# Kernel optimization log

Measured on AMD Instinct MI355X. Metric: run time of the kernel, lower is better.

## Reference

```python
import jax, jax.numpy as jnp
import numpy as np

DIM = 4096
N_HEAD = 32
N_KV_HEAD = 8
HEAD_DIM = DIM // N_HEAD  # 128
B, T = 2, 2048


def _rope_freqs(T, head_dim, theta=10000.0):
    inv = 1.0 / (theta ** (np.arange(0, head_dim, 2, dtype=np.float32) / head_dim))
    t = np.arange(T, dtype=np.float32)
    ang = np.outer(t, inv)  # [T, head_dim/2]
    return jnp.asarray(np.stack([np.cos(ang), np.sin(ang)], axis=-1))  # [T, hd/2, 2]


def setup_inputs() -> dict:
    key = jax.random.key(0)
    ks = jax.random.split(key, 5)
    s = 1.0 / np.sqrt(DIM)
    return {
        "x": jax.random.normal(ks[0], (B, T, DIM), dtype=jnp.float32),
        "freqs_cis": _rope_freqs(T, HEAD_DIM),
        "wq": jax.random.normal(ks[1], (DIM, N_HEAD * HEAD_DIM), dtype=jnp.float32) * s,
        "wk": jax.random.normal(ks[2], (DIM, N_KV_HEAD * HEAD_DIM), dtype=jnp.float32) * s,
        "wv": jax.random.normal(ks[3], (DIM, N_KV_HEAD * HEAD_DIM), dtype=jnp.float32) * s,
        "wo": jax.random.normal(ks[4], (DIM, DIM), dtype=jnp.float32) * s,
    }


def _apply_rotary(x, freqs_cis):
    # x: [B, T, H, head_dim]; freqs_cis: [T, head_dim/2, 2]
    xs = x.reshape(*x.shape[:-1], -1, 2)  # [B, T, H, hd/2, 2]
    fc = freqs_cis[None, :, None, :, :]   # [1, T, 1, hd/2, 2]
    real = xs[..., 0] * fc[..., 0] - xs[..., 1] * fc[..., 1]
    imag = xs[..., 1] * fc[..., 0] + xs[..., 0] * fc[..., 1]
    return jnp.stack([real, imag], axis=-1).reshape(x.shape)


def reference(x, freqs_cis, wq, wk, wv, wo):
    Bx, Tx, C = x.shape
    q = (x @ wq).reshape(Bx, Tx, N_HEAD, HEAD_DIM)
    k = (x @ wk).reshape(Bx, Tx, N_KV_HEAD, HEAD_DIM)
    v = (x @ wv).reshape(Bx, Tx, N_KV_HEAD, HEAD_DIM)
    q = _apply_rotary(q, freqs_cis)
    k = _apply_rotary(k, freqs_cis)
    # [B, H, T, hd]
    q = q.transpose(0, 2, 1, 3)
    k = k.transpose(0, 2, 1, 3)
    v = v.transpose(0, 2, 1, 3)
    # GQA: expand kv heads to match query heads
    rep = N_HEAD // N_KV_HEAD
    k = jnp.repeat(k, rep, axis=1)
    v = jnp.repeat(v, rep, axis=1)
    scale = 1.0 / np.sqrt(HEAD_DIM)
    scores = jnp.einsum("bhqd,bhkd->bhqk", q, k) * scale
    causal = jnp.tril(jnp.ones((Tx, Tx), dtype=bool))
    scores = jnp.where(causal[None, None], scores, jnp.float32(-1e30))
    attn = jax.nn.softmax(scores, axis=-1)
    y = jnp.einsum("bhqk,bhkd->bhqd", attn, v)
    y = y.transpose(0, 2, 1, 3).reshape(Bx, Tx, C)
    return y @ wo
```

## Files before the change

### kernel.cpp

```cpp
#include <hip/hip_runtime.h>

#define DIM  4096
#define NH   32
#define NKV  8
#define HD   128
#define BSZ  2
#define TSEQ 2048

typedef __bf16 bf16x8 __attribute__((ext_vector_type(8)));
typedef unsigned short ushort8v __attribute__((ext_vector_type(8)));
typedef float f32x4 __attribute__((ext_vector_type(4)));

typedef void GV __attribute__((address_space(1)));
typedef void LV __attribute__((address_space(3)));

__device__ __forceinline__ unsigned short f2bf(float f) {
  unsigned u = __builtin_bit_cast(unsigned, f);
  u += 0x7FFFu + ((u >> 16) & 1u);
  return (unsigned short)(u >> 16);
}
__device__ __forceinline__ float bf2f(unsigned short b) {
  unsigned u = ((unsigned)b) << 16;
  return __builtin_bit_cast(float, u);
}
__device__ __forceinline__ void gload16(const unsigned short* g, unsigned short* l) {
  __builtin_amdgcn_global_load_lds((GV*)g, (LV*)l, 16, 0, 0);
}
__device__ __forceinline__ f32x4 mfma16(bf16x8 a, bf16x8 b, f32x4 c) {
  return __builtin_amdgcn_mfma_f32_16x16x32_bf16(a, b, c, 0, 0, 0);
}
__device__ __forceinline__ bf16x8 lds8(const unsigned short* p) {
  return __builtin_bit_cast(bf16x8, *(const ushort8v*)p);
}

__global__ void detect_dtype(const unsigned int* __restrict__ fc, int* __restrict__ flag) {
  if (threadIdx.x == 0 && blockIdx.x == 0)
    *flag = (fc[0] == 0x3F800000u) ? 0 : 1;
}

__global__ void cast_x(const void* __restrict__ src, unsigned short* __restrict__ dst,
                       const int* __restrict__ flag) {
  long t = (long)blockIdx.x * 256 + threadIdx.x;
  if (*flag) {
    ((uint2*)dst)[t] = ((const uint2*)src)[t];
  } else {
    float4 f = ((const float4*)src)[t];
    ushort4 o;
    o.x = f2bf(f.x); o.y = f2bf(f.y); o.z = f2bf(f.z); o.w = f2bf(f.w);
    ((ushort4*)dst)[t] = o;
  }
}

__global__ __launch_bounds__(256) void transpose64(const void* __restrict__ src,
                                                   unsigned short* __restrict__ dst,
                                                   int R, int C, const int* __restrict__ flag) {
  __shared__ unsigned short tile[64][68];
  const int isbf = *flag;
  const int tid = threadIdx.x;
  const int c0g = blockIdx.x * 64, r0g = blockIdx.y * 64;
  const int cc = (tid & 15) * 4;
  if (isbf) {
    const unsigned short* s = (const unsigned short*)src;
#pragma unroll
    for (int it = 0; it < 4; ++it) {
      const int r = it * 16 + (tid >> 4);
      ushort4 v = *(const ushort4*)(s + (long)(r0g + r) * C + c0g + cc);
      *(ushort4*)&tile[r][cc] = v;
    }
  } else {
    const float* s = (const float*)src;
#pragma unroll
    for (int it = 0; it < 4; ++it) {
      const int r = it * 16 + (tid >> 4);
      float4 f = *(const float4*)(s + (long)(r0g + r) * C + c0g + cc);
      ushort4 v;
      v.x = f2bf(f.x); v.y = f2bf(f.y); v.z = f2bf(f.z); v.w = f2bf(f.w);
      *(ushort4*)&tile[r][cc] = v;
    }
  }
  __syncthreads();
#pragma unroll
  for (int it = 0; it < 2; ++it) {
    const int c = (tid >> 3) + it * 32;
    const int r0 = (tid & 7) * 8;
    ushort8v o;
#pragma unroll
    for (int u = 0; u < 8; ++u) o[u] = tile[r0 + u][c];
    *(ushort8v*)(dst + (long)(c0g + c) * R + r0g + r0) = o;
  }
}

__device__ __forceinline__ void gemm128_loop(const unsigned short* __restrict__ A,
                                             const unsigned short* __restrict__ Bt,
                                             unsigned short* As, unsigned short* Bs,
                                             long tileM, long tileN, f32x4 (&acc)[4][4]) {
  const int tid = (int)threadIdx.x;
  const int lane = tid & 63, wave = tid >> 6;
  const int wr = wave >> 1, wc = wave & 1;
  const int lm = lane & 15, quad = lane >> 4;
  const int sr = tid >> 3;
  const int schunk = ((tid & 7) ^ (sr & 7)) * 8;
  const unsigned short* Ag = A + (tileM + sr) * 4096L + schunk;
  const unsigned short* Bg = Bt + (tileN + sr) * 4096L + schunk;
  unsigned short* Al = As + sr * 64 + (tid & 7) * 8;
  unsigned short* Bl = Bs + sr * 64 + (tid & 7) * 8;

  auto stgA = [&](int slot, int half, int tt) {
    const unsigned short* g = Ag + (long)half * (64 * 4096L) + (long)tt * 64;
    unsigned short* l = Al + slot * 8192 + half * 4096;
    gload16(g, l);
    gload16(g + 32 * 4096L, l + 2048);
  };
  auto stgB = [&](int slot, int half, int tt) {
    const unsigned short* g = Bg + (long)half * (64 * 4096L) + (long)tt * 64;
    unsigned short* l = Bl + slot * 8192 + half * 4096;
    gload16(g, l);
    gload16(g + 32 * 4096L, l + 2048);
  };
  auto rdA = [&](int so, int f, int kk) {
    return lds8(&As[so + (wr * 64 + f * 16 + lm) * 64 + (((kk * 4 + quad) ^ (lm & 7)) * 8)]);
  };
  auto rdB = [&](int so, int f, int kk) {
    return lds8(&Bs[so + (wc * 64 + f * 16 + lm) * 64 + (((kk * 4 + quad) ^ (lm & 7)) * 8)]);
  };

  stgB(0, 0, 0); stgB(0, 1, 0); stgA(0, 0, 0); stgA(0, 1, 0);
  stgB(1, 0, 1); stgB(1, 1, 1); stgA(1, 0, 1);
  asm volatile("s_waitcnt vmcnt(6)" ::: "memory");
  __builtin_amdgcn_sched_barrier(0);
  __builtin_amdgcn_s_barrier();

#pragma unroll 2
  for (int t = 0; t < 64; ++t) {
    __builtin_amdgcn_sched_barrier(0);
    const int s = t & 1;
    const int so = s * 8192;
    bf16x8 a[4][2], b[4][2];
#pragma unroll
    for (int f = 0; f < 4; ++f) { a[f][0] = rdA(so, f, 0); a[f][1] = rdA(so, f, 1); }
#pragma unroll
    for (int f = 0; f < 4; ++f) { b[f][0] = rdB(so, f, 0); b[f][1] = rdB(so, f, 1); }
    if (t < 63) stgA(s ^ 1, 1, t + 1);
    asm volatile("s_waitcnt lgkmcnt(0)" ::: "memory");
    __builtin_amdgcn_sched_barrier(0);
    __builtin_amdgcn_s_setprio(1);
#pragma unroll
    for (int mf = 0; mf < 4; ++mf)
#pragma unroll
      for (int nf = 0; nf < 4; ++nf)
        acc[mf][nf] = mfma16(a[mf][0], b[nf][0], acc[mf][nf]);
    __builtin_amdgcn_s_setprio(0);
    __builtin_amdgcn_sched_barrier(0);
    __builtin_amdgcn_s_barrier();
    if (t < 62) { stgB(s, 0, t + 2); stgB(s, 1, t + 2); stgA(s, 0, t + 2); }
    __builtin_amdgcn_s_setprio(1);
#pragma unroll
    for (int mf = 0; mf < 4; ++mf)
#pragma unroll
      for (int nf = 0; nf < 4; ++nf)
        acc[mf][nf] = mfma16(a[mf][1], b[nf][1], acc[mf][nf]);
    __builtin_amdgcn_s_setprio(0);
    if (t < 62)       asm volatile("s_waitcnt vmcnt(6)" ::: "memory");
    else if (t == 62) asm volatile("s_waitcnt vmcnt(0)" ::: "memory");
    __builtin_amdgcn_sched_barrier(0);
    __builtin_amdgcn_s_barrier();
  }
}

__global__ __launch_bounds__(256, 2) void gemm_qkv8(const unsigned short* __restrict__ A,
                                                    const unsigned short* __restrict__ Bt,
                                                    const void* __restrict__ fcv,
                                                    const int* __restrict__ flag,
                                                    unsigned short* __restrict__ qo,
                                                    unsigned short* __restrict__ ko,
                                                    unsigned short* __restrict__ vo) {
  __shared__ __align__(16) unsigned short As[2 * 8192];
  __shared__ __align__(16) unsigned short Bs[2 * 8192];
  const int bid = (int)blockIdx.x;
  const int nb2 = (bid & 7) * 192 + (bid >> 3);
  const long tileM = (long)(nb2 / 48) * 128;
  const long tileN = (long)(nb2 % 48) * 128;
  f32x4 acc[4][4] = {};
  gemm128_loop(A, Bt, As, Bs, tileM, tileN, acc);
  const int tid = (int)threadIdx.x;
  const int lane = tid & 63, wave = tid >> 6;
  const int wr = wave >> 1, wc = wave & 1;
  const int lm = lane & 15, quad = lane >> 4;
  const int isbf = *flag;
  const int nb = (int)tileN + wc * 64;
  if (nb < 5120) {
    const int isk = (nb >= 4096);
    unsigned short* dst = isk ? ko : qo;
    const int hpb = isk ? NKV : NH;
    const int coff = isk ? 4096 : 0;
#pragma unroll
    for (int mf = 0; mf < 4; ++mf)
#pragma unroll
      for (int r = 0; r < 4; ++r) {
        const int m = (int)tileM + wr * 64 + mf * 16 + quad * 4 + r;
        const int b = m >> 11, tq = m & (TSEQ - 1);
#pragma unroll
        for (int nf = 0; nf < 4; ++nf) {
          const int n = nb + nf * 16 + lm;
          float val = acc[mf][nf][r];
          float par = __shfl_xor(val, 1);
          const int ip = (n & 127) >> 1;
          const long fo = (long)tq * 64 + ip;
          float cz, sz;
          if (isbf) {
            const unsigned short* fu = (const unsigned short*)fcv;
            cz = bf2f(fu[fo * 2]); sz = bf2f(fu[fo * 2 + 1]);
          } else {
            float2 cs = ((const float2*)fcv)[fo];
            cz = cs.x; sz = cs.y;
          }
          float out = (n & 1) ? (val * cz + par * sz) : (val * cz - par * sz);
          const int h = (n - coff) >> 7, d = n & 127;
          dst[((long)(b * hpb + h) * TSEQ + tq) * HD + d] = f2bf(out);
        }
      }
  } else {
#pragma unroll
    for (int mf = 0; mf < 4; ++mf)
#pragma unroll
      for (int r = 0; r < 4; ++r) {
        const int m = (int)tileM + wr * 64 + mf * 16 + quad * 4 + r;
        const int b = m >> 11, tq = m & (TSEQ - 1);
#pragma unroll
        for (int nf = 0; nf < 4; ++nf) {
          const int n = nb + nf * 16 + lm;
          const int h = (n - 5120) >> 7, d = n & 127;
          vo[((long)(b * NKV + h) * HD + d) * TSEQ + tq] = f2bf(acc[mf][nf][r]);
        }
      }
  }
}

__global__ __launch_bounds__(256, 2) void gemm_wo8(const unsigned short* __restrict__ A,
                                                   const unsigned short* __restrict__ Bt,
                                                   void* __restrict__ Cv,
                                                   const int* __restrict__ flag) {
  __shared__ __align__(16) unsigned short As[2 * 8192];
  __shared__ __align__(16) unsigned short Bs[2 * 8192];
  const int bid = (int)blockIdx.x;
  const int nb2 = (bid & 7) * 128 + (bid >> 3);
  const long tileM = (long)(nb2 >> 5) * 128;
  const long tileN = (long)(nb2 & 31) * 128;
  f32x4 acc[4][4] = {};
  gemm128_loop(A, Bt, As, Bs, tileM, tileN, acc);
  const int tid = (int)threadIdx.x;
  const int lane = tid & 63, wave = tid >> 6;
  const int wr = wave >> 1, wc = wave & 1;
  const int lm = lane & 15, quad = lane >> 4;
  const int obf = *flag;
  const long N = 4096;
  if (obf) {
    unsigned short* C = (unsigned short*)Cv;
#pragma unroll
    for (int mf = 0; mf < 4; ++mf)
#pragma unroll
      for (int nf = 0; nf < 4; ++nf)
#pragma unroll
        for (int r = 0; r < 4; ++r)
          C[(tileM + wr * 64 + mf * 16 + quad * 4 + r) * N + tileN + wc * 64 + nf * 16 + lm] =
              f2bf(acc[mf][nf][r]);
  } else {
    float* C = (float*)Cv;
#pragma unroll
    for (int mf = 0; mf < 4; ++mf)
#pragma unroll
      for (int nf = 0; nf < 4; ++nf)
#pragma unroll
        for (int r = 0; r < 4; ++r)
          C[(tileM + wr * 64 + mf * 16 + quad * 4 + r) * N + tileN + wc * 64 + nf * 16 + lm] =
              acc[mf][nf][r];
  }
}

__global__ __launch_bounds__(256, 3) void flash_attn(const unsigned short* __restrict__ q,
                                                     const unsigned short* __restrict__ k,
                                                     const unsigned short* __restrict__ vT,
                                                     unsigned short* __restrict__ y) {
  __shared__ unsigned short Ks[2][32 * 128];
  __shared__ unsigned short Vs[2][128 * 32];
  __shared__ unsigned short Pl[4][32 * 40];
  const int tid = threadIdx.x;
  const int lane = tid & 63, wave = tid >> 6;
  const int lm = lane & 15, quad = lane >> 4;
  const int bh = blockIdx.y, b = bh >> 5, h = bh & 31, kvh = h >> 2;
  const int pr = (int)blockIdx.x;
  const unsigned short* Kb = k + (long)(b * NKV + kvh) * TSEQ * HD;
  const unsigned short* Vb = vT + (long)(b * NKV + kvh) * HD * TSEQ;
  const float scale = 0.08838834764831845f;
  const int krow = tid >> 4, kcl = ((tid & 15) ^ (krow & 7)) * 8;
  const int vrow = tid >> 2, vcl = ((tid & 3) ^ ((vrow >> 1) & 3)) * 8;

  for (int seg = 0; seg < 2; ++seg) {
    const int qi = seg ? (15 - pr) : pr;
    const int q0 = qi * 128;
    const unsigned short* Qb = q + ((long)(b * NH + h) * TSEQ + q0 + wave * 32) * HD;
    bf16x8 qf[2][4];
#pragma unroll
    for (int mi = 0; mi < 2; ++mi)
#pragma unroll
      for (int ks = 0; ks < 4; ++ks)
        qf[mi][ks] = __builtin_bit_cast(bf16x8,
            *(const ushort8v*)(Qb + (mi * 16 + lm) * HD + ks * 32 + quad * 8));
    f32x4 o[2][8] = {};
    float li[2][4] = {};
    const int ktiles = qi * 4 + 4;
    if (seg) __syncthreads();
    {
      gload16(Kb + krow * HD + kcl, &Ks[0][tid * 8]);
      gload16(Kb + (16 + krow) * HD + kcl, &Ks[0][2048 + tid * 8]);
      gload16(Vb + (long)vrow * TSEQ + vcl, &Vs[0][tid * 8]);
      gload16(Vb + (long)(64 + vrow) * TSEQ + vcl, &Vs[0][2048 + tid * 8]);
    }
    for (int kt = 0; kt < ktiles; ++kt) {
      __syncthreads();
      if (kt + 1 < ktiles) {
        const int bi = (kt + 1) & 1;
        const unsigned short* Kg = Kb + (long)(kt + 1) * 32 * HD;
        gload16(Kg + krow * HD + kcl, &Ks[bi][tid * 8]);
        gload16(Kg + (16 + krow) * HD + kcl, &Ks[bi][2048 + tid * 8]);
        const unsigned short* Vg = Vb + (kt + 1) * 32;
        gload16(Vg + (long)vrow * TSEQ + vcl, &Vs[bi][tid * 8]);
        gload16(Vg + (long)(64 + vrow) * TSEQ + vcl, &Vs[bi][2048 + tid * 8]);
      }
      const unsigned short* KsB = Ks[kt & 1];
      const unsigned short* VsB = Vs[kt & 1];
      f32x4 s[2][2] = {};
#pragma unroll
      for (int ni = 0; ni < 2; ++ni)
#pragma unroll
        for (int ks = 0; ks < 4; ++ks) {
          bf16x8 kf = lds8(&KsB[(ni * 16 + lm) * 128 + ((ks * 4 + quad) ^ (lm & 7)) * 8]);
          s[0][ni] = mfma16(qf[0][ks], kf, s[0][ni]);
          s[1][ni] = mfma16(qf[1][ks], kf, s[1][ni]);
        }
      unsigned short* PlW = &Pl[wave][0];
#pragma unroll
      for (int mi = 0; mi < 2; ++mi)
#pragma unroll
        for (int r = 0; r < 4; ++r) {
          const int qg = q0 + wave * 32 + mi * 16 + quad * 4 + r;
#pragma unroll
          for (int ni = 0; ni < 2; ++ni) {
            const int kg = kt * 32 + ni * 16 + lm;
            float p = (kg <= qg) ? __expf(s[mi][ni][r] * scale) : 0.f;
            li[mi][r] += p;
            PlW[(mi * 16 + quad * 4 + r) * 40 + ni * 16 + lm] = f2bf(p);
          }
        }
      bf16x8 pf0 = lds8(&PlW[lm * 40 + quad * 8]);
      bf16x8 pf1 = lds8(&PlW[(16 + lm) * 40 + quad * 8]);
#pragma unroll
      for (int db = 0; db < 8; ++db) {
        bf16x8 vf = lds8(&VsB[(db * 16 + lm) * 32 + (quad ^ ((lm >> 1) & 3)) * 8]);
        o[0][db] = mfma16(pf0, vf, o[0][db]);
        o[1][db] = mfma16(pf1, vf, o[1][db]);
      }
    }
    float inv[2][4];
#pragma unroll
    for (int mi = 0; mi < 2; ++mi)
#pragma unroll
      for (int r = 0; r < 4; ++r) {
        float l = li[mi][r];
        l += __shfl_xor(l, 1, 16);
        l += __shfl_xor(l, 2, 16);
        l += __shfl_xor(l, 4, 16);
        l += __shfl_xor(l, 8, 16);
        inv[mi][r] = 1.0f / l;
      }
    unsigned short* yo = y + ((long)b * TSEQ + q0 + wave * 32) * DIM + h * 128 + lm;
#pragma unroll
    for (int mi = 0; mi < 2; ++mi)
#pragma unroll
      for (int r = 0; r < 4; ++r) {
        unsigned short* yr = yo + (long)(mi * 16 + quad * 4 + r) * DIM;
#pragma unroll
        for (int db = 0; db < 8; ++db)
          yr[db * 16] = f2bf(o[mi][db][r] * inv[mi][r]);
      }
  }
}

extern "C" void kernel_launch(void* const* d_in, const int* in_sizes, int n_in,
                              void* d_out, int out_size, void* d_ws, size_t ws_size,
                              hipStream_t stream) {
  const void* x  = d_in[0];
  const void* fc = d_in[1];
  const void* wq = d_in[2];
  const void* wk = d_in[3];
  const void* wv = d_in[4];
  const void* wo = d_in[5];
  char* ws = (char*)d_ws;
  int* flag             = (int*)ws;
  unsigned short* xb    = (unsigned short*)(ws + 256);
  unsigned short* wqkvT = xb + 16777216L;
  unsigned short* woT   = wqkvT + 25165824L;
  unsigned short* qb    = woT + 16777216L;
  unsigned short* kb    = qb + 16777216L;
  unsigned short* vb    = kb + 4194304L;
  unsigned short* yb    = xb;

  detect_dtype<<<dim3(1), dim3(64), 0, stream>>>((const unsigned int*)fc, flag);
  cast_x<<<dim3(16384), dim3(256), 0, stream>>>(x, xb, flag);
  transpose64<<<dim3(64, 64), dim3(256), 0, stream>>>(wq, wqkvT, 4096, 4096, flag);
  transpose64<<<dim3(16, 64), dim3(256), 0, stream>>>(wk, wqkvT + 4096L * 4096, 4096, 1024, flag);
  transpose64<<<dim3(16, 64), dim3(256), 0, stream>>>(wv, wqkvT + 5120L * 4096, 4096, 1024, flag);
  transpose64<<<dim3(64, 64), dim3(256), 0, stream>>>(wo, woT, 4096, 4096, flag);
  gemm_qkv8<<<dim3(1536), dim3(256), 0, stream>>>(xb, wqkvT, fc, flag, qb, kb, vb);
  flash_attn<<<dim3(8, 64), dim3(256), 0, stream>>>(qb, kb, vb, yb);
  gemm_wo8<<<dim3(1024), dim3(256), 0, stream>>>(yb, woT, d_out, flag);
}
```

Before: 773.9 us.

## Remap GEMM tiles per XCD and enlarge flash attention blocks to 256 queries

The two projection GEMMs now assign tiles so that each XCD works on a compact 8x8 group of M/N tiles within a band, aiming for better L2 reuse of A and B panels. Flash attention moves from 256-thread blocks that each process two paired 128-row query tiles to 512-thread blocks that each own a 256-row query tile. The larger block shares each K/V tile load across eight waves, halving K/V traffic per query. Causal load balancing changes from pairing tiles inside a block to ordering blocks longest-first, and the larger block may reduce occupancy and raise barrier cost.

```diff
diff --git a/kernel.cpp b/kernel.cpp
--- a/kernel.cpp
+++ b/kernel.cpp
@@ -177,9 +177,11 @@
   __shared__ __align__(16) unsigned short As[2 * 8192];
   __shared__ __align__(16) unsigned short Bs[2 * 8192];
   const int bid = (int)blockIdx.x;
-  const int nb2 = (bid & 7) * 192 + (bid >> 3);
-  const long tileM = (long)(nb2 / 48) * 128;
-  const long tileN = (long)(nb2 % 48) * 128;
+  const int xcd = bid & 7, idx = bid >> 3;
+  const int band = idx >> 6;
+  const int rr = idx & 63;
+  const long tileM = (long)((xcd & 3) * 8 + (rr & 7)) * 128;
+  const long tileN = (long)((xcd >> 2) * 24 + band * 8 + (rr >> 3)) * 128;
   f32x4 acc[4][4] = {};
   gemm128_loop(A, Bt, As, Bs, tileM, tileN, acc);
   const int tid = (int)threadIdx.x;
@@ -243,9 +245,11 @@
   __shared__ __align__(16) unsigned short As[2 * 8192];
   __shared__ __align__(16) unsigned short Bs[2 * 8192];
   const int bid = (int)blockIdx.x;
-  const int nb2 = (bid & 7) * 128 + (bid >> 3);
-  const long tileM = (long)(nb2 >> 5) * 128;
-  const long tileN = (long)(nb2 & 31) * 128;
+  const int xcd = bid & 7, idx = bid >> 3;
+  const int band = idx >> 6;
+  const int rr = idx & 63;
+  const long tileM = (long)((xcd & 3) * 8 + (rr & 7)) * 128;
+  const long tileN = (long)((xcd >> 2) * 16 + band * 8 + (rr >> 3)) * 128;
   f32x4 acc[4][4] = {};
   gemm128_loop(A, Bt, As, Bs, tileM, tileN, acc);
   const int tid = (int)threadIdx.x;
@@ -277,113 +281,107 @@
   }
 }
 
-__global__ __launch_bounds__(256, 3) void flash_attn(const unsigned short* __restrict__ q,
+__global__ __launch_bounds__(512, 2) void flash_attn(const unsigned short* __restrict__ q,
                                                      const unsigned short* __restrict__ k,
                                                      const unsigned short* __restrict__ vT,
                                                      unsigned short* __restrict__ y) {
   __shared__ unsigned short Ks[2][32 * 128];
   __shared__ unsigned short Vs[2][128 * 32];
-  __shared__ unsigned short Pl[4][32 * 40];
+  __shared__ unsigned short Pl[8][32 * 40];
   const int tid = threadIdx.x;
   const int lane = tid & 63, wave = tid >> 6;
   const int lm = lane & 15, quad = lane >> 4;
-  const int bh = blockIdx.y, b = bh >> 5, h = bh & 31, kvh = h >> 2;
-  const int pr = (int)blockIdx.x;
+  const int bid = (int)blockIdx.x;
+  const int halfg = bid >> 8, jj = bid & 255;
+  const int qt = jj >> 6, bh = jj & 63;
+  const int qi = halfg ? qt : 7 - qt;
+  const int b = bh >> 5, h = bh & 31, kvh = h >> 2;
+  const int q0 = qi * 256;
   const unsigned short* Kb = k + (long)(b * NKV + kvh) * TSEQ * HD;
   const unsigned short* Vb = vT + (long)(b * NKV + kvh) * HD * TSEQ;
+  const unsigned short* Qb = q + ((long)(b * NH + h) * TSEQ + q0 + wave * 32) * HD;
+  bf16x8 qf[2][4];
+#pragma unroll
+  for (int mi = 0; mi < 2; ++mi)
+#pragma unroll
+    for (int ks = 0; ks < 4; ++ks)
+      qf[mi][ks] = __builtin_bit_cast(bf16x8,
+          *(const ushort8v*)(Qb + (mi * 16 + lm) * HD + ks * 32 + quad * 8));
+  f32x4 o[2][8] = {};
+  float li[2][4] = {};
   const float scale = 0.08838834764831845f;
   const int krow = tid >> 4, kcl = ((tid & 15) ^ (krow & 7)) * 8;
   const int vrow = tid >> 2, vcl = ((tid & 3) ^ ((vrow >> 1) & 3)) * 8;
-
-  for (int seg = 0; seg < 2; ++seg) {
-    const int qi = seg ? (15 - pr) : pr;
-    const int q0 = qi * 128;
-    const unsigned short* Qb = q + ((long)(b * NH + h) * TSEQ + q0 + wave * 32) * HD;
-    bf16x8 qf[2][4];
+  const int ktiles = qi * 8 + 8;
+  {
+    gload16(Kb + krow * HD + kcl, &Ks[0][tid * 8]);
+    gload16(Vb + (long)vrow * TSEQ + vcl, &Vs[0][tid * 8]);
+  }
+  for (int kt = 0; kt < ktiles; ++kt) {
+    __syncthreads();
+    if (kt + 1 < ktiles) {
+      const int bi = (kt + 1) & 1;
+      const unsigned short* Kg = Kb + (long)(kt + 1) * 32 * HD;
+      gload16(Kg + krow * HD + kcl, &Ks[bi][tid * 8]);
+      const unsigned short* Vg = Vb + (kt + 1) * 32;
+      gload16(Vg + (long)vrow * TSEQ + vcl, &Vs[bi][tid * 8]);
+    }
+    const unsigned short* KsB = Ks[kt & 1];
+    const unsigned short* VsB = Vs[kt & 1];
+    f32x4 s[2][2] = {};
+#pragma unroll
+    for (int ni = 0; ni < 2; ++ni)
+#pragma unroll
+      for (int ks = 0; ks < 4; ++ks) {
+        bf16x8 kf = lds8(&KsB[(ni * 16 + lm) * 128 + ((ks * 4 + quad) ^ (lm & 7)) * 8]);
+        s[0][ni] = mfma16(qf[0][ks], kf, s[0][ni]);
+        s[1][ni] = mfma16(qf[1][ks], kf, s[1][ni]);
+      }
+    unsigned short* PlW = &Pl[wave][0];
 #pragma unroll
     for (int mi = 0; mi < 2; ++mi)
 #pragma unroll
-      for (int ks = 0; ks < 4; ++ks)
-        qf[mi][ks] = __builtin_bit_cast(bf16x8,
-            *(const ushort8v*)(Qb + (mi * 16 + lm) * HD + ks * 32 + quad * 8));
-    f32x4 o[2][8] = {};
-    float li[2][4] = {};
-    const int ktiles = qi * 4 + 4;
-    if (seg) __syncthreads();
-    {
-      gload16(Kb + krow * HD + kcl, &Ks[0][tid * 8]);
-      gload16(Kb + (16 + krow) * HD + kcl, &Ks[0][2048 + tid * 8]);
-      gload16(Vb + (long)vrow * TSEQ + vcl, &Vs[0][tid * 8]);
-      gload16(Vb + (long)(64 + vrow) * TSEQ + vcl, &Vs[0][2048 + tid * 8]);
-    }
-    for (int kt = 0; kt < ktiles; ++kt) {
-      __syncthreads();
-      if (kt + 1 < ktiles) {
-        const int bi = (kt + 1) & 1;
-        const unsigned short* Kg = Kb + (long)(kt + 1) * 32 * HD;
-        gload16(Kg + krow * HD + kcl, &Ks[bi][tid * 8]);
-        gload16(Kg + (16 + krow) * HD + kcl, &Ks[bi][2048 + tid * 8]);
-        const unsigned short* Vg = Vb + (kt + 1) * 32;
-        gload16(Vg + (long)vrow * TSEQ + vcl, &Vs[bi][tid * 8]);
-        gload16(Vg + (long)(64 + vrow) * TSEQ + vcl, &Vs[bi][2048 + tid * 8]);
+      for (int r = 0; r < 4; ++r) {
+        const int qg = q0 + wave * 32 + mi * 16 + quad * 4 + r;
+#pragma unroll
+        for (int ni = 0; ni < 2; ++ni) {
+          const int kg = kt * 32 + ni * 16 + lm;
+          float p = (kg <= qg) ? __expf(s[mi][ni][r] * scale) : 0.f;
+          li[mi][r] += p;
+          PlW[(mi * 16 + quad * 4 + r) * 40 + ni * 16 + lm] = f2bf(p);
+        }
       }
-      const unsigned short* KsB = Ks[kt & 1];
-      const unsigned short* VsB = Vs[kt & 1];
-      f32x4 s[2][2] = {};
-#pragma unroll
-      for (int ni = 0; ni < 2; ++ni)
-#pragma unroll
-        for (int ks = 0; ks < 4; ++ks) {
-          bf16x8 kf = lds8(&KsB[(ni * 16 + lm) * 128 + ((ks * 4 + quad) ^ (lm & 7)) * 8]);
-          s[0][ni] = mfma16(qf[0][ks], kf, s[0][ni]);
-          s[1][ni] = mfma16(qf[1][ks], kf, s[1][ni]);
-        }
-      unsigned short* PlW = &Pl[wave][0];
-#pragma unroll
-      for (int mi = 0; mi < 2; ++mi)
-#pragma unroll
-        for (int r = 0; r < 4; ++r) {
-          const int qg = q0 + wave * 32 + mi * 16 + quad * 4 + r;
-#pragma unroll
-          for (int ni = 0; ni < 2; ++ni) {
-            const int kg = kt * 32 + ni * 16 + lm;
-            float p = (kg <= qg) ? __expf(s[mi][ni][r] * scale) : 0.f;
-            li[mi][r] += p;
-            PlW[(mi * 16 + quad * 4 + r) * 40 + ni * 16 + lm] = f2bf(p);
-          }
-        }
-      bf16x8 pf0 = lds8(&PlW[lm * 40 + quad * 8]);
-      bf16x8 pf1 = lds8(&PlW[(16 + lm) * 40 + quad * 8]);
-#pragma unroll
-      for (int db = 0; db < 8; ++db) {
-        bf16x8 vf = lds8(&VsB[(db * 16 + lm) * 32 + (quad ^ ((lm >> 1) & 3)) * 8]);
-        o[0][db] = mfma16(pf0, vf, o[0][db]);
-        o[1][db] = mfma16(pf1, vf, o[1][db]);
-      }
-    }
-    float inv[2][4];
-#pragma unroll
-    for (int mi = 0; mi < 2; ++mi)
-#pragma unroll
-      for (int r = 0; r < 4; ++r) {
-        float l = li[mi][r];
-        l += __shfl_xor(l, 1, 16);
-        l += __shfl_xor(l, 2, 16);
-        l += __shfl_xor(l, 4, 16);
-        l += __shfl_xor(l, 8, 16);
-        inv[mi][r] = 1.0f / l;
-      }
-    unsigned short* yo = y + ((long)b * TSEQ + q0 + wave * 32) * DIM + h * 128 + lm;
-#pragma unroll
-    for (int mi = 0; mi < 2; ++mi)
-#pragma unroll
-      for (int r = 0; r < 4; ++r) {
-        unsigned short* yr = yo + (long)(mi * 16 + quad * 4 + r) * DIM;
-#pragma unroll
-        for (int db = 0; db < 8; ++db)
-          yr[db * 16] = f2bf(o[mi][db][r] * inv[mi][r]);
-      }
-  }
+    bf16x8 pf0 = lds8(&PlW[lm * 40 + quad * 8]);
+    bf16x8 pf1 = lds8(&PlW[(16 + lm) * 40 + quad * 8]);
+#pragma unroll
+    for (int db = 0; db < 8; ++db) {
+      bf16x8 vf = lds8(&VsB[(db * 16 + lm) * 32 + (quad ^ ((lm >> 1) & 3)) * 8]);
+      o[0][db] = mfma16(pf0, vf, o[0][db]);
+      o[1][db] = mfma16(pf1, vf, o[1][db]);
+    }
+  }
+  float inv[2][4];
+#pragma unroll
+  for (int mi = 0; mi < 2; ++mi)
+#pragma unroll
+    for (int r = 0; r < 4; ++r) {
+      float l = li[mi][r];
+      l += __shfl_xor(l, 1, 16);
+      l += __shfl_xor(l, 2, 16);
+      l += __shfl_xor(l, 4, 16);
+      l += __shfl_xor(l, 8, 16);
+      inv[mi][r] = 1.0f / l;
+    }
+  unsigned short* yo = y + ((long)b * TSEQ + q0 + wave * 32) * DIM + h * 128 + lm;
+#pragma unroll
+  for (int mi = 0; mi < 2; ++mi)
+#pragma unroll
+    for (int r = 0; r < 4; ++r) {
+      unsigned short* yr = yo + (long)(mi * 16 + quad * 4 + r) * DIM;
+#pragma unroll
+      for (int db = 0; db < 8; ++db)
+        yr[db * 16] = f2bf(o[mi][db][r] * inv[mi][r]);
+    }
 }
 
 extern "C" void kernel_launch(void* const* d_in, const int* in_sizes, int n_in,
@@ -412,6 +410,6 @@
   transpose64<<<dim3(16, 64), dim3(256), 0, stream>>>(wv, wqkvT + 5120L * 4096, 4096, 1024, flag);
   transpose64<<<dim3(64, 64), dim3(256), 0, stream>>>(wo, woT, 4096, 4096, flag);
   gemm_qkv8<<<dim3(1536), dim3(256), 0, stream>>>(xb, wqkvT, fc, flag, qb, kb, vb);
-  flash_attn<<<dim3(8, 64), dim3(256), 0, stream>>>(qb, kb, vb, yb);
+  flash_attn<<<dim3(512), dim3(512), 0, stream>>>(qb, kb, vb, yb);
   gemm_wo8<<<dim3(1024), dim3(256), 0, stream>>>(yb, woT, d_out, flag);
 }
```

Result: faster. 734.2 us (-5.1%).
